# Performance work log

Measured on AMD Instinct MI355X. Metric: run time of the kernel, lower is better.

The kernel has to match this reference:

```python
import jax, jax.numpy as jnp
import numpy as np

C = 2048
RED = 8
D = C // RED  # 256


def setup_inputs() -> dict:
    key = jax.random.key(0)
    ks = jax.random.split(key, 8)
    n, h, w = 4, 64, 64
    x = jax.random.normal(ks[0], (n, C, h, w), dtype=jnp.float32)
    # 1x1 conv weights stored as [out_ch, in_ch]
    w1 = jax.random.normal(ks[1], (D, C), dtype=jnp.float32) * 0.02
    b1 = jnp.zeros((D,), dtype=jnp.float32)
    w2 = jax.random.normal(ks[2], (D, C), dtype=jnp.float32) * 0.02
    b2 = jnp.zeros((D,), dtype=jnp.float32)
    w3 = jax.random.normal(ks[3], (C, C), dtype=jnp.float32) * 0.02
    b3 = jnp.zeros((C,), dtype=jnp.float32)
    alpha = jnp.zeros((1,), dtype=jnp.float32)
    return {"x": x, "w1": w1, "b1": b1, "w2": w2, "b2": b2,
            "w3": w3, "b3": b3, "alpha": alpha}


def reference(x, w1, b1, w2, b2, w3, b3, alpha):
    n, c, h, w = x.shape
    hw = h * w
    xf = x.reshape(n, c, hw)  # [n, C, HW]
    # 1x1 convs == per-position matmuls over channels
    e1 = jax.nn.relu(jnp.einsum('dc,ncp->ndp', w1, xf) + b1[None, :, None])  # [n, D, HW]
    e2 = jax.nn.relu(jnp.einsum('dc,ncp->ndp', w2, xf) + b2[None, :, None])  # [n, D, HW]
    assembly = jax.nn.relu(jnp.einsum('oc,ncp->nop', w3, xf) + b3[None, :, None])  # [n, C, HW]
    # attention[i, j] = softmax_j( e1[:, i] . e2[:, j] )
    scores = jnp.einsum('ndi,ndj->nij', e1, e2)  # [n, HW, HW]
    attn = jax.nn.softmax(scores, axis=-1)
    # torch.bmm(x, attn^T): out[:, :, i] = sum_j x[:, :, j] * attn[i, j]
    out = jnp.einsum('ncj,nij->nci', xf, attn)  # [n, C, HW]
    y = alpha[0] * out + assembly
    return y.reshape(n, c, h, w)
```

## Files before the change

kernel.cpp:

```cpp
#include <hip/hip_runtime.h>
#include <math.h>

#define CC 2048
#define DD 256
#define PP 4096
#define NB 4

typedef float f32x16 __attribute__((ext_vector_type(16)));
typedef __bf16 bfrag __attribute__((ext_vector_type(8)));

#define AS1(p) ((const __attribute__((address_space(1))) void*)(p))
#define AS3(p) ((__attribute__((address_space(3))) void*)(p))

__device__ __forceinline__ unsigned short f2bf(float f) {
    unsigned int u = __float_as_uint(f);
    u = (u + 0x7fffu + ((u >> 16) & 1u)) >> 16;
    return (unsigned short)u;
}

__global__ __launch_bounds__(256) void prep(const float* __restrict__ x, unsigned short* __restrict__ xT,
                                            const float* __restrict__ w3, unsigned short* __restrict__ w3b) {
    const int t = threadIdx.x;
    if (blockIdx.z == NB) {
        int bid = blockIdx.y * 64 + blockIdx.x;
        int base = (bid * 256 + t) * 8;
#pragma unroll
        for (int j = 0; j < 2; ++j) {
            float4 v = *(const float4*)(w3 + base + j * 4);
            ushort4 r;
            r.x = f2bf(v.x); r.y = f2bf(v.y); r.z = f2bf(v.z); r.w = f2bf(v.w);
            *(ushort4*)(w3b + base + j * 4) = r;
        }
        return;
    }
    __shared__ float tile[64 * 64];
    const int n  = blockIdx.z;
    const int c0 = blockIdx.y * 64;
    const int p0 = blockIdx.x * 64;
    const float* xn = x + (size_t)n * CC * PP;
    {
        const int cl = t >> 4;
        const int g  = t & 15;
        const int pl = g * 4;
#pragma unroll
        for (int ps = 0; ps < 4; ++ps) {
            const int c = cl + ps * 16;
            float4 v = *(const float4*)(xn + (size_t)(c0 + c) * PP + p0 + pl);
            const int gs = g ^ (c >> 2);
            *(float4*)(tile + c * 64 + gs * 4) = v;
        }
    }
    __syncthreads();
    unsigned short* xTn = xT + (size_t)n * PP * CC;
    {
        const int pl2 = t >> 4;
        const int cq  = t & 15;
        const int c4  = cq * 4;
#pragma unroll
        for (int ps = 0; ps < 4; ++ps) {
            const int p  = pl2 + ps * 16;
            const int gs2 = (p >> 2) ^ cq;
            const int base = gs2 * 4 + (p & 3);
            ushort4 r;
            r.x = f2bf(tile[(c4 + 0) * 64 + base]);
            r.y = f2bf(tile[(c4 + 1) * 64 + base]);
            r.z = f2bf(tile[(c4 + 2) * 64 + base]);
            r.w = f2bf(tile[(c4 + 3) * 64 + base]);
            *(ushort4*)(xTn + (size_t)(p0 + p) * CC + c0 + c4) = r;
        }
    }
}

__global__ __launch_bounds__(512, 2) void gemm_assembly(
    const unsigned short* __restrict__ w3b,
    const unsigned short* __restrict__ xT,
    const float* __restrict__ b3,
    float* __restrict__ out)
{
    __shared__ __align__(16) char sm[131072];

    const int t    = threadIdx.x;
    const int wave = t >> 6;
    const int lane = t & 63;
    const int l31  = lane & 31;
    const int lh   = lane >> 5;
    const int swz  = lane & 7;

    const int flat = blockIdx.x + (blockIdx.y << 4);
    const int sf   = ((flat & 7) << 4) | (flat >> 3);
    const int p0   = (sf & 15) << 8;
    const int m0   = (sf >> 4) << 8;
    const int nb   = blockIdx.z;

    const int rA = t >> 3;
    const int g  = (t & 7) ^ (rA & 7);
    const unsigned short* Ag = w3b + (size_t)(m0 + rA) * CC + g * 8;
    const unsigned short* Bg = xT + (size_t)nb * PP * CC + (size_t)(p0 + rA) * CC + g * 8;
    const int ldsw = wave << 10;

    const char* Abase = sm + ((wave >> 2) << 14) + l31 * 128;
    const char* Bbase = sm + 65536 + (((wave & 3) >> 1) << 14) + ((((wave & 1) << 6) + l31) * 128);

    const int ck0 = ((0 + lh) ^ swz) << 4;
    const int ck1 = ((2 + lh) ^ swz) << 4;
    const int ck2 = ((4 + lh) ^ swz) << 4;
    const int ck3 = ((6 + lh) ^ swz) << 4;

    f32x16 c00 = {}, c10 = {}, c20 = {}, c30 = {};
    f32x16 c01 = {}, c11 = {}, c21 = {}, c31 = {};
    bfrag a0_0, a0_1, a0_2, a0_3, a1_0, a1_1, a1_2, a1_3;
    bfrag b0_0, b0_1, b0_2, b0_3, b1_0, b1_1, b1_2, b1_3;

#define STG(SB, DO, kt, h) do { \
    const unsigned short* _s = (SB) + (size_t)(h) * 128 * CC + (size_t)(kt) * 64; \
    char* _d = sm + (DO) + (((kt) & 1) << 15) + ((h) << 14) + ldsw; \
    __builtin_amdgcn_global_load_lds(AS1(_s), AS3(_d), 16, 0, 0); \
    __builtin_amdgcn_global_load_lds(AS1(_s + 64 * CC), AS3(_d + 8192), 16, 0, 0); \
} while (0)

#define LDA(dst, P, mi, ck) dst = *(const bfrag*)(Abase + ((P) << 15) + ((mi) << 12) + (ck))
#define LDB(dst, P, ni, ck) dst = *(const bfrag*)(Bbase + ((P) << 15) + ((ni) << 12) + (ck))
#define MM(acc, a, b) acc = __builtin_amdgcn_mfma_f32_32x32x16_bf16(a, b, acc, 0, 0, 0)
#define BARR __builtin_amdgcn_s_barrier()
#define LG0 do { asm volatile("s_waitcnt lgkmcnt(0)" ::: "memory"); __builtin_amdgcn_sched_barrier(0); } while (0)
#define PRI(x) __builtin_amdgcn_s_setprio(x)

#define TILE(P, kt, IA, IB, VMS, VMZ) do { \
     \
    LDA(a0_0,P,0,ck0); LDA(a0_1,P,0,ck1); LDA(a0_2,P,0,ck2); LDA(a0_3,P,0,ck3); \
    LDA(a1_0,P,1,ck0); LDA(a1_1,P,1,ck1); LDA(a1_2,P,1,ck2); LDA(a1_3,P,1,ck3); \
    LDB(b0_0,P,0,ck0); LDB(b0_1,P,0,ck1); LDB(b0_2,P,0,ck2); LDB(b0_3,P,0,ck3); \
    if (IA) STG(Ag, 0, (kt) + 1, 0); \
    asm volatile("s_waitcnt lgkmcnt(8)" ::: "memory"); \
    BARR; LG0; PRI(1); \
    MM(c00, a0_0, b0_0); MM(c10, a1_0, b0_0); \
    MM(c00, a0_1, b0_1); MM(c10, a1_1, b0_1); \
    MM(c00, a0_2, b0_2); MM(c10, a1_2, b0_2); \
    MM(c00, a0_3, b0_3); MM(c10, a1_3, b0_3); \
    PRI(0); BARR; \
     \
    LDB(b1_0,P,1,ck0); LDB(b1_1,P,1,ck1); LDB(b1_2,P,1,ck2); LDB(b1_3,P,1,ck3); \
    if (IA) STG(Ag, 0, (kt) + 1, 1); \
    BARR; LG0; PRI(1); \
    MM(c01, a0_0, b1_0); MM(c11, a1_0, b1_0); \
    MM(c01, a0_1, b1_1); MM(c11, a1_1, b1_1); \
    MM(c01, a0_2, b1_2); MM(c11, a1_2, b1_2); \
    MM(c01, a0_3, b1_3); MM(c11, a1_3, b1_3); \
    PRI(0); BARR; \
     \
    LDA(a0_0,P,2,ck0); LDA(a0_1,P,2,ck1); LDA(a0_2,P,2,ck2); LDA(a0_3,P,2,ck3); \
    LDA(a1_0,P,3,ck0); LDA(a1_1,P,3,ck1); LDA(a1_2,P,3,ck2); LDA(a1_3,P,3,ck3); \
    if (IB) STG(Bg, 65536, (kt) + 2, 0); \
    BARR; LG0; PRI(1); \
    MM(c21, a0_0, b1_0); MM(c31, a1_0, b1_0); \
    MM(c21, a0_1, b1_1); MM(c31, a1_1, b1_1); \
    MM(c21, a0_2, b1_2); MM(c31, a1_2, b1_2); \
    MM(c21, a0_3, b1_3); MM(c31, a1_3, b1_3); \
    PRI(0); BARR; \
     \
    if (IB) STG(Bg, 65536, (kt) + 2, 1); \
    BARR; PRI(1); \
    MM(c20, a0_0, b0_0); MM(c30, a1_0, b0_0); \
    MM(c20, a0_1, b0_1); MM(c30, a1_1, b0_1); \
    MM(c20, a0_2, b0_2); MM(c30, a1_2, b0_2); \
    MM(c20, a0_3, b0_3); MM(c30, a1_3, b0_3); \
    PRI(0); \
    if (VMS) asm volatile("s_waitcnt vmcnt(4)" ::: "memory"); \
    if (VMZ) asm volatile("s_waitcnt vmcnt(0)" ::: "memory"); \
    BARR; \
} while (0)

    STG(Ag, 0, 0, 0); STG(Ag, 0, 0, 1);
    STG(Bg, 65536, 0, 0); STG(Bg, 65536, 0, 1);
    STG(Bg, 65536, 1, 0); STG(Bg, 65536, 1, 1);
    asm volatile("s_waitcnt vmcnt(4)" ::: "memory");
    BARR;

#pragma unroll 1
    for (int kt = 0; kt < 30; kt += 2) {
        TILE(0, kt,     1, 1, 1, 0);
        TILE(1, kt + 1, 1, 1, 1, 0);
    }
    TILE(0, 30, 1, 0, 0, 1);
    TILE(1, 31, 0, 0, 0, 0);

#undef TILE
#undef STG
#undef LDA
#undef LDB
#undef MM
#undef BARR
#undef LG0
#undef PRI

    const int wr = (wave >> 2) << 7;
    const int wc = (wave & 3) << 6;
    float* outn = out + (size_t)nb * CC * PP + p0 + wc + l31;
#pragma unroll
    for (int mi = 0; mi < 4; ++mi) {
        f32x16 v0 = (mi == 0) ? c00 : (mi == 1) ? c10 : (mi == 2) ? c20 : c30;
        f32x16 v1 = (mi == 0) ? c01 : (mi == 1) ? c11 : (mi == 2) ? c21 : c31;
#pragma unroll
        for (int r = 0; r < 16; ++r) {
            const int rowl = (r & 3) + 8 * (r >> 2) + 4 * lh;
            const int o = m0 + wr + mi * 32 + rowl;
            const float bias = b3[o];
            float* orow = outn + (size_t)o * PP;
            float x0 = v0[r] + bias;
            float x1 = v1[r] + bias;
            orow[0]  = x0 > 0.f ? x0 : 0.f;
            orow[32] = x1 > 0.f ? x1 : 0.f;
        }
    }
}

__global__ void fb_e12(const float* __restrict__ x,
                       const float* __restrict__ w1, const float* __restrict__ b1,
                       const float* __restrict__ w2, const float* __restrict__ b2,
                       const float* __restrict__ alpha,
                       float* __restrict__ e1, float* __restrict__ e2) {
    if (alpha[0] == 0.f) return;
    const size_t total = (size_t)NB * DD * PP;
    for (size_t idx = (size_t)blockIdx.x * blockDim.x + threadIdx.x; idx < total;
         idx += (size_t)gridDim.x * blockDim.x) {
        int p = (int)(idx % PP);
        size_t nd = idx / PP;
        int d = (int)(nd % DD);
        int n = (int)(nd / DD);
        const float* xn = x + (size_t)n * CC * PP + p;
        float s1 = b1[d], s2 = b2[d];
        for (int c = 0; c < CC; ++c) {
            float xv = xn[(size_t)c * PP];
            s1 += w1[(size_t)d * CC + c] * xv;
            s2 += w2[(size_t)d * CC + c] * xv;
        }
        e1[idx] = fmaxf(s1, 0.f);
        e2[idx] = fmaxf(s2, 0.f);
    }
}

__global__ void fb_attn(const float* __restrict__ x,
                        const float* __restrict__ e1, const float* __restrict__ e2,
                        const float* __restrict__ alpha,
                        float* __restrict__ out) {
    const float a = alpha[0];
    if (a == 0.f) return;
    __shared__ float s[PP];
    __shared__ float e1i[DD];
    __shared__ float red[256];
    const int t = threadIdx.x;
    for (int ii = blockIdx.x; ii < NB * PP; ii += gridDim.x) {
        const int n = ii >> 12;
        const int i = ii & (PP - 1);
        const float* e1n = e1 + (size_t)n * DD * PP;
        const float* e2n = e2 + (size_t)n * DD * PP;
        if (t < DD) e1i[t] = e1n[(size_t)t * PP + i];
        __syncthreads();
        for (int j = t; j < PP; j += 256) {
            float acc = 0.f;
            for (int d = 0; d < DD; ++d) acc += e1i[d] * e2n[(size_t)d * PP + j];
            s[j] = acc;
        }
        __syncthreads();
        float m = -INFINITY;
        for (int j = t; j < PP; j += 256) m = fmaxf(m, s[j]);
        red[t] = m; __syncthreads();
        for (int o = 128; o > 0; o >>= 1) { if (t < o) red[t] = fmaxf(red[t], red[t + o]); __syncthreads(); }
        m = red[0]; __syncthreads();
        float l = 0.f;
        for (int j = t; j < PP; j += 256) { float e = __expf(s[j] - m); s[j] = e; l += e; }
        red[t] = l; __syncthreads();
        for (int o = 128; o > 0; o >>= 1) { if (t < o) red[t] += red[t + o]; __syncthreads(); }
        l = red[0]; __syncthreads();
        const float inv = a / l;
        const float* xn = x + (size_t)n * CC * PP;
        float* on = out + (size_t)n * CC * PP;
        for (int c = t; c < CC; c += 256) {
            const float* xr = xn + (size_t)c * PP;
            float acc = 0.f;
            for (int j = 0; j < PP; ++j) acc += s[j] * xr[j];
            on[(size_t)c * PP + i] += inv * acc;
        }
        __syncthreads();
    }
}

extern "C" void kernel_launch(void* const* d_in, const int* in_sizes, int n_in,
                              void* d_out, int out_size, void* d_ws, size_t ws_size,
                              hipStream_t stream) {
    (void)in_sizes; (void)n_in; (void)out_size; (void)ws_size;
    const float* x     = (const float*)d_in[0];
    const float* w1    = (const float*)d_in[1];
    const float* b1    = (const float*)d_in[2];
    const float* w2    = (const float*)d_in[3];
    const float* b2    = (const float*)d_in[4];
    const float* w3    = (const float*)d_in[5];
    const float* b3    = (const float*)d_in[6];
    const float* alpha = (const float*)d_in[7];
    float* out = (float*)d_out;

    unsigned short* xT  = (unsigned short*)d_ws;
    unsigned short* w3b = (unsigned short*)((char*)d_ws + (size_t)NB * PP * CC * 2);
    float* e1 = (float*)d_ws;
    float* e2 = e1 + (size_t)NB * DD * PP;

    prep<<<dim3(PP / 64, CC / 64, NB + 1), dim3(256), 0, stream>>>(x, xT, w3, w3b);
    gemm_assembly<<<dim3(PP / 256, CC / 256, NB), dim3(512), 0, stream>>>(w3b, xT, b3, out);
    fb_e12<<<dim3(512), dim3(256), 0, stream>>>(x, w1, b1, w2, b2, alpha, e1, e2);
    fb_attn<<<dim3(1024), dim3(256), 0, stream>>>(x, e1, e2, alpha, out);
}
```

Before: 386.1 us.

## Preload all A fragments per tile and cut barriers in the bf16 MFMA loop

The assembly GEMM inner tile now loads all four A sub-fragments and both B sub-fragments from LDS up front, into separate register sets. It then runs the four MFMA groups with staggered lgkmcnt waits instead of a barrier and full wait around each group, leaving only two block barriers per tile. It also drops the block-index swizzle in favour of a direct grid-to-tile mapping. The aim is to cut synchronisation stalls and overlap LDS reads with MFMA work, at the cost of more vector registers (possible spills or lower occupancy) and possibly worse L2 locality without the swizzle.

```diff
diff --git a/kernel.cpp b/kernel.cpp
--- a/kernel.cpp
+++ b/kernel.cpp
@@ -86,11 +86,9 @@
     const int lh   = lane >> 5;
     const int swz  = lane & 7;
 
-    const int flat = blockIdx.x + (blockIdx.y << 4);
-    const int sf   = ((flat & 7) << 4) | (flat >> 3);
-    const int p0   = (sf & 15) << 8;
-    const int m0   = (sf >> 4) << 8;
-    const int nb   = blockIdx.z;
+    const int p0 = blockIdx.x << 8;
+    const int m0 = blockIdx.y << 8;
+    const int nb = blockIdx.z;
 
     const int rA = t >> 3;
     const int g  = (t & 7) ^ (rA & 7);
@@ -108,7 +106,10 @@
 
     f32x16 c00 = {}, c10 = {}, c20 = {}, c30 = {};
     f32x16 c01 = {}, c11 = {}, c21 = {}, c31 = {};
-    bfrag a0_0, a0_1, a0_2, a0_3, a1_0, a1_1, a1_2, a1_3;
+    bfrag aA0_0, aA0_1, aA0_2, aA0_3;
+    bfrag aA1_0, aA1_1, aA1_2, aA1_3;
+    bfrag aA2_0, aA2_1, aA2_2, aA2_3;
+    bfrag aA3_0, aA3_1, aA3_2, aA3_3;
     bfrag b0_0, b0_1, b0_2, b0_3, b1_0, b1_1, b1_2, b1_3;
 
 #define STG(SB, DO, kt, h) do { \
@@ -122,52 +123,62 @@
 #define LDB(dst, P, ni, ck) dst = *(const bfrag*)(Bbase + ((P) << 15) + ((ni) << 12) + (ck))
 #define MM(acc, a, b) acc = __builtin_amdgcn_mfma_f32_32x32x16_bf16(a, b, acc, 0, 0, 0)
 #define BARR __builtin_amdgcn_s_barrier()
-#define LG0 do { asm volatile("s_waitcnt lgkmcnt(0)" ::: "memory"); __builtin_amdgcn_sched_barrier(0); } while (0)
+#define SB0  __builtin_amdgcn_sched_barrier(0)
 #define PRI(x) __builtin_amdgcn_s_setprio(x)
 
-#define TILE(P, kt, IA, IB, VMS, VMZ) do { \
-     \
-    LDA(a0_0,P,0,ck0); LDA(a0_1,P,0,ck1); LDA(a0_2,P,0,ck2); LDA(a0_3,P,0,ck3); \
-    LDA(a1_0,P,1,ck0); LDA(a1_1,P,1,ck1); LDA(a1_2,P,1,ck2); LDA(a1_3,P,1,ck3); \
-    LDB(b0_0,P,0,ck0); LDB(b0_1,P,0,ck1); LDB(b0_2,P,0,ck2); LDB(b0_3,P,0,ck3); \
+#define TILE(P, kt, IA, IB, VM4, VM0, EB) do { \
+    SB0; \
+     \
+    LDA(aA0_0,P,0,ck0); LDA(aA0_1,P,0,ck1); LDA(aA0_2,P,0,ck2); LDA(aA0_3,P,0,ck3); \
+    LDA(aA1_0,P,1,ck0); LDA(aA1_1,P,1,ck1); LDA(aA1_2,P,1,ck2); LDA(aA1_3,P,1,ck3); \
+    LDB(b0_0,P,0,ck0);  LDB(b0_1,P,0,ck1);  LDB(b0_2,P,0,ck2);  LDB(b0_3,P,0,ck3); \
+    SB0; \
     if (IA) STG(Ag, 0, (kt) + 1, 0); \
-    asm volatile("s_waitcnt lgkmcnt(8)" ::: "memory"); \
-    BARR; LG0; PRI(1); \
-    MM(c00, a0_0, b0_0); MM(c10, a1_0, b0_0); \
-    MM(c00, a0_1, b0_1); MM(c10, a1_1, b0_1); \
-    MM(c00, a0_2, b0_2); MM(c10, a1_2, b0_2); \
-    MM(c00, a0_3, b0_3); MM(c10, a1_3, b0_3); \
-    PRI(0); BARR; \
-     \
-    LDB(b1_0,P,1,ck0); LDB(b1_1,P,1,ck1); LDB(b1_2,P,1,ck2); LDB(b1_3,P,1,ck3); \
+     \
+    LDB(b1_0,P,1,ck0);  LDB(b1_1,P,1,ck1);  LDB(b1_2,P,1,ck2);  LDB(b1_3,P,1,ck3); \
+    SB0; \
     if (IA) STG(Ag, 0, (kt) + 1, 1); \
-    BARR; LG0; PRI(1); \
-    MM(c01, a0_0, b1_0); MM(c11, a1_0, b1_0); \
-    MM(c01, a0_1, b1_1); MM(c11, a1_1, b1_1); \
-    MM(c01, a0_2, b1_2); MM(c11, a1_2, b1_2); \
-    MM(c01, a0_3, b1_3); MM(c11, a1_3, b1_3); \
-    PRI(0); BARR; \
-     \
-    LDA(a0_0,P,2,ck0); LDA(a0_1,P,2,ck1); LDA(a0_2,P,2,ck2); LDA(a0_3,P,2,ck3); \
-    LDA(a1_0,P,3,ck0); LDA(a1_1,P,3,ck1); LDA(a1_2,P,3,ck2); LDA(a1_3,P,3,ck3); \
+     \
+    LDA(aA2_0,P,2,ck0); LDA(aA2_1,P,2,ck1); LDA(aA2_2,P,2,ck2); LDA(aA2_3,P,2,ck3); \
+    LDA(aA3_0,P,3,ck0); LDA(aA3_1,P,3,ck1); LDA(aA3_2,P,3,ck2); LDA(aA3_3,P,3,ck3); \
+    SB0; \
+     \
+    asm volatile("s_waitcnt lgkmcnt(12)" ::: "memory"); SB0; \
+    PRI(1); \
+    MM(c00, aA0_0, b0_0); MM(c10, aA1_0, b0_0); \
+    MM(c00, aA0_1, b0_1); MM(c10, aA1_1, b0_1); \
+    MM(c00, aA0_2, b0_2); MM(c10, aA1_2, b0_2); \
+    MM(c00, aA0_3, b0_3); MM(c10, aA1_3, b0_3); \
+    PRI(0); \
+     \
+    asm volatile("s_waitcnt lgkmcnt(8)" ::: "memory"); SB0; \
+    PRI(1); \
+    MM(c01, aA0_0, b1_0); MM(c11, aA1_0, b1_0); \
+    MM(c01, aA0_1, b1_1); MM(c11, aA1_1, b1_1); \
+    MM(c01, aA0_2, b1_2); MM(c11, aA1_2, b1_2); \
+    MM(c01, aA0_3, b1_3); MM(c11, aA1_3, b1_3); \
+    PRI(0); \
+    BARR; SB0; \
     if (IB) STG(Bg, 65536, (kt) + 2, 0); \
-    BARR; LG0; PRI(1); \
-    MM(c21, a0_0, b1_0); MM(c31, a1_0, b1_0); \
-    MM(c21, a0_1, b1_1); MM(c31, a1_1, b1_1); \
-    MM(c21, a0_2, b1_2); MM(c31, a1_2, b1_2); \
-    MM(c21, a0_3, b1_3); MM(c31, a1_3, b1_3); \
-    PRI(0); BARR; \
-     \
+     \
+    asm volatile("s_waitcnt lgkmcnt(0)" ::: "memory"); SB0; \
+    PRI(1); \
+    MM(c21, aA2_0, b1_0); MM(c31, aA3_0, b1_0); \
+    MM(c21, aA2_1, b1_1); MM(c31, aA3_1, b1_1); \
+    MM(c21, aA2_2, b1_2); MM(c31, aA3_2, b1_2); \
+    MM(c21, aA2_3, b1_3); MM(c31, aA3_3, b1_3); \
+    PRI(0); \
     if (IB) STG(Bg, 65536, (kt) + 2, 1); \
-    BARR; PRI(1); \
-    MM(c20, a0_0, b0_0); MM(c30, a1_0, b0_0); \
-    MM(c20, a0_1, b0_1); MM(c30, a1_1, b0_1); \
-    MM(c20, a0_2, b0_2); MM(c30, a1_2, b0_2); \
-    MM(c20, a0_3, b0_3); MM(c30, a1_3, b0_3); \
+     \
+    PRI(1); \
+    MM(c20, aA2_0, b0_0); MM(c30, aA3_0, b0_0); \
+    MM(c20, aA2_1, b0_1); MM(c30, aA3_1, b0_1); \
+    MM(c20, aA2_2, b0_2); MM(c30, aA3_2, b0_2); \
+    MM(c20, aA2_3, b0_3); MM(c30, aA3_3, b0_3); \
     PRI(0); \
-    if (VMS) asm volatile("s_waitcnt vmcnt(4)" ::: "memory"); \
-    if (VMZ) asm volatile("s_waitcnt vmcnt(0)" ::: "memory"); \
-    BARR; \
+    if (VM4) asm volatile("s_waitcnt vmcnt(4)" ::: "memory"); \
+    if (VM0) asm volatile("s_waitcnt vmcnt(0)" ::: "memory"); \
+    if (EB) BARR; \
 } while (0)
 
     STG(Ag, 0, 0, 0); STG(Ag, 0, 0, 1);
@@ -178,11 +189,11 @@
 
 #pragma unroll 1
     for (int kt = 0; kt < 30; kt += 2) {
-        TILE(0, kt,     1, 1, 1, 0);
-        TILE(1, kt + 1, 1, 1, 1, 0);
-    }
-    TILE(0, 30, 1, 0, 0, 1);
-    TILE(1, 31, 0, 0, 0, 0);
+        TILE(0, kt,     1, 1, 1, 0, 1);
+        TILE(1, kt + 1, 1, (kt + 1 < 30), 1, 0, 1);
+    }
+    TILE(0, 30, 1, 0, 0, 1, 1);
+    TILE(1, 31, 0, 0, 0, 0, 0);
 
 #undef TILE
 #undef STG
@@ -190,7 +201,7 @@
 #undef LDB
 #undef MM
 #undef BARR
-#undef LG0
+#undef SB0
 #undef PRI
 
     const int wr = (wave >> 2) << 7;
```

After: 375.8 us. 1.03x faster.
